# Performance work log

Hardware: AMD Instinct MI355X
Metric: run time of the kernel (lower is better)

## Reference

```python
import jax, jax.numpy as jnp
import numpy as np

EMB_DIM = 300
TEMPERATURE = 0.01
REWEIGHT = True
N = 8192
NUM_GROUPS = 100


def setup_inputs() -> dict:
    key = jax.random.key(0)
    ks = jax.random.split(key, 6)
    s = 1.0 / np.sqrt(EMB_DIM)
    x = jax.random.normal(ks[0], (N, EMB_DIM), dtype=jnp.float32)
    W1 = jax.random.normal(ks[1], (EMB_DIM, EMB_DIM), dtype=jnp.float32) * s
    b1 = jnp.zeros((EMB_DIM,), dtype=jnp.float32)
    W2 = jax.random.normal(ks[2], (EMB_DIM, EMB_DIM), dtype=jnp.float32) * s
    b2 = jnp.zeros((EMB_DIM,), dtype=jnp.float32)
    # labels in [1, 100]: all > 0 so the group_y>0 filter keeps every row
    labels = jax.random.randint(ks[3], (N,), 1, NUM_GROUPS + 1, dtype=jnp.int32)
    return {"x": x, "W1": W1, "b1": b1, "W2": W2, "b2": b2, "labels": labels}


def reference(x, W1, b1, W2, b2, labels):
    # projector: Linear -> ReLU -> Linear
    h = jax.nn.relu(x @ W1 + b1) @ W2 + b2
    # L2 normalize rows
    f = h / jnp.linalg.norm(h, axis=1, keepdims=True)
    # pairwise similarity / temperature, row-max subtracted (detached)
    logits = (f @ f.T) / TEMPERATURE                      # [N, N]
    logits = logits - jax.lax.stop_gradient(jnp.max(logits, axis=1, keepdims=True))

    lab = labels[:, None]
    mask = (lab == lab.T).astype(logits.dtype)            # same-group mask
    logits_mask = 1.0 - jnp.eye(mask.shape[0], dtype=logits.dtype)  # drop diagonal
    mask = mask * logits_mask

    # rows with at least one positive (torch filters these; we weight instead)
    pos_count = jnp.sum(mask, axis=1)                     # [N]
    valid = pos_count > 0

    if REWEIGHT:
        pos_m = logits_mask * mask
        neg_m = logits_mask * (1.0 - mask)
        pos_sum = jnp.sum(pos_m, axis=1, keepdims=True)
        neg_sum = jnp.sum(neg_m, axis=1, keepdims=True)
        log_pos = jnp.where(pos_sum > 0, jnp.log(jnp.maximum(pos_sum, 1.0)), 0.0)
        log_neg = jnp.where(neg_sum > 0, jnp.log(jnp.maximum(neg_sum, 1.0)), 0.0)
        logits = (logits - log_pos) * pos_m + (logits - log_neg) * neg_m

    exp_logits = jnp.exp(logits) * logits_mask
    log_prob = logits - jnp.log(jnp.sum(exp_logits, axis=1, keepdims=True))
    mean_log_prob_pos = jnp.sum(mask * log_prob, axis=1) / jnp.where(valid, pos_count, 1.0)
    validf = valid.astype(logits.dtype)
    loss = -TEMPERATURE * jnp.sum(mean_log_prob_pos * validf) / jnp.sum(validf)
    return loss
```

## Files before the change

### kernel.cpp

```cpp
#include <hip/hip_runtime.h>
#include <hip/hip_bf16.h>


#define N_ROWS 8192
#define D_PAD 320
#define NG 100
#define TEMP 0.01f
#define NSPLIT 32
#define JCHUNK (N_ROWS / NSPLIT)
#define LOG2E100 144.2695041f

typedef short short8v __attribute__((ext_vector_type(8)));
typedef float float4v __attribute__((ext_vector_type(4)));

__device__ __forceinline__ short f2bf(float f) {
  union { __hip_bfloat16 h; short s; } u;
  u.h = __float2bfloat16(f);
  return u.s;
}

__global__ __launch_bounds__(256) void setup_kernel(
    const float* __restrict__ W1, const float* __restrict__ W2,
    const int* __restrict__ labels,
    __hip_bfloat16* __restrict__ w1t, __hip_bfloat16* __restrict__ w2t,
    int* __restrict__ counts)
{
  __shared__ int hc[NG + 1];
  int b = blockIdx.x, tid = threadIdx.x;
  if (b < 800) {
    int isW2 = (b >= 400);
    int idx = (b - (isW2 ? 400 : 0)) * 256 + tid;
    const float* W = isW2 ? W2 : W1;
    __hip_bfloat16* dst = isW2 ? w2t : w1t;
    int n = idx / D_PAD, k = idx - n * D_PAD;
    float v = (n < 300 && k < 300) ? W[(size_t)k * 300 + n] : 0.0f;
    dst[idx] = __float2bfloat16(v);
  } else {
    if (tid <= NG) hc[tid] = 0;
    __syncthreads();
    int row = (b - 800) * 256 + tid;
    atomicAdd(&hc[labels[row]], 1);
    __syncthreads();
    if (tid <= NG && hc[tid] > 0) atomicAdd(&counts[tid], hc[tid]);
  }
}

__global__ __launch_bounds__(256, 2) void mlp_fused_kernel(
    const float* __restrict__ x, const __hip_bfloat16* __restrict__ w1t,
    const __hip_bfloat16* __restrict__ w2t, const float* __restrict__ b1,
    const float* __restrict__ b2, __hip_bfloat16* __restrict__ fb)
{
  __shared__ __align__(16) short Ws[64 * D_PAD];
  __shared__ __align__(16) short H1[64 * D_PAD];
  int tid = threadIdx.x;
  int lane = tid & 63, wave = tid >> 6;
  int g = lane >> 4, lc = lane & 15, sw = lc & 7;
  int i0 = blockIdx.x * 64;

  short8v afr[10];
  {
    const float* xp = x + (size_t)(i0 + wave * 16 + lc) * 300;
#pragma unroll
    for (int kk = 0; kk < 10; ++kk) {
      int k0 = kk * 32 + g * 8;
      short8v v;
      if (k0 + 8 <= 300) {
        float4 a = *(const float4*)(xp + k0);
        float4 c = *(const float4*)(xp + k0 + 4);
        v[0] = f2bf(a.x); v[1] = f2bf(a.y); v[2] = f2bf(a.z); v[3] = f2bf(a.w);
        v[4] = f2bf(c.x); v[5] = f2bf(c.y); v[6] = f2bf(c.z); v[7] = f2bf(c.w);
      } else if (k0 < 300) {
        float4 a = *(const float4*)(xp + k0);
        v[0] = f2bf(a.x); v[1] = f2bf(a.y); v[2] = f2bf(a.z); v[3] = f2bf(a.w);
        v[4] = 0; v[5] = 0; v[6] = 0; v[7] = 0;
      } else {
        v = short8v{0, 0, 0, 0, 0, 0, 0, 0};
      }
      afr[kk] = v;
    }
  }

  for (int c = 0; c < 5; ++c) {
    __syncthreads();
    {
      const int4* src = (const int4*)w1t;
      int4* dst = (int4*)Ws;
#pragma unroll
      for (int t = 0; t < 10; ++t) {
        int e = tid + t * 256;
        int r = e / 40, q = e - r * 40;
        dst[r * 40 + (q ^ (r & 7))] = src[(size_t)(c * 64 + r) * 40 + q];
      }
    }
    __syncthreads();
    for (int js = 0; js < 4; ++js) {
      float4v acc = {0.f, 0.f, 0.f, 0.f};
      const short* rowp = Ws + (js * 16 + lc) * D_PAD;
#pragma unroll
      for (int kk = 0; kk < 10; ++kk) {
        short8v bf = *(const short8v*)(rowp + (((g + 4 * kk) ^ sw) << 3));
        acc = __builtin_amdgcn_mfma_f32_16x16x32_bf16(afr[kk], bf, acc, 0, 0, 0);
      }
      int n = c * 64 + js * 16 + lc;
      float bv = (n < 300) ? b1[n] : 0.0f;
#pragma unroll
      for (int r = 0; r < 4; ++r) {
        int row = wave * 16 + g * 4 + r;
        int q = n >> 3;
        H1[row * D_PAD + ((q ^ (row & 7)) << 3) + (n & 7)] =
            f2bf(fmaxf(acc[r] + bv, 0.0f));
      }
    }
  }
  __syncthreads();

  short8v hfr[10];
  {
    const short* rp = H1 + (wave * 16 + lc) * D_PAD;
#pragma unroll
    for (int kk = 0; kk < 10; ++kk)
      hfr[kk] = *(const short8v*)(rp + (((g + 4 * kk) ^ sw) << 3));
  }

  float4v h2a[5][4];
  for (int c = 0; c < 5; ++c) {
    __syncthreads();
    {
      const int4* src = (const int4*)w2t;
      int4* dst = (int4*)Ws;
#pragma unroll
      for (int t = 0; t < 10; ++t) {
        int e = tid + t * 256;
        int r = e / 40, q = e - r * 40;
        dst[r * 40 + (q ^ (r & 7))] = src[(size_t)(c * 64 + r) * 40 + q];
      }
    }
    __syncthreads();
#pragma unroll
    for (int js = 0; js < 4; ++js) {
      float4v acc = {0.f, 0.f, 0.f, 0.f};
      const short* rowp = Ws + (js * 16 + lc) * D_PAD;
#pragma unroll
      for (int kk = 0; kk < 10; ++kk) {
        short8v bf = *(const short8v*)(rowp + (((g + 4 * kk) ^ sw) << 3));
        acc = __builtin_amdgcn_mfma_f32_16x16x32_bf16(hfr[kk], bf, acc, 0, 0, 0);
      }
      int n = c * 64 + js * 16 + lc;
      float bv = (n < 300) ? b2[n] : 0.0f;
#pragma unroll
      for (int r = 0; r < 4; ++r) acc[r] += bv;
      h2a[c][js] = acc;
    }
  }

  float ssq[4] = {0.f, 0.f, 0.f, 0.f};
#pragma unroll
  for (int c = 0; c < 5; ++c)
#pragma unroll
    for (int js = 0; js < 4; ++js)
#pragma unroll
      for (int r = 0; r < 4; ++r) ssq[r] = fmaf(h2a[c][js][r], h2a[c][js][r], ssq[r]);
  for (int m = 1; m < 16; m <<= 1)
#pragma unroll
    for (int r = 0; r < 4; ++r) ssq[r] += __shfl_xor(ssq[r], m, 64);
  float inv[4];
#pragma unroll
  for (int r = 0; r < 4; ++r) inv[r] = rsqrtf(ssq[r]);
#pragma unroll
  for (int c = 0; c < 5; ++c)
#pragma unroll
    for (int js = 0; js < 4; ++js) {
      int n = c * 64 + js * 16 + lc;
#pragma unroll
      for (int r = 0; r < 4; ++r) {
        int row = i0 + wave * 16 + g * 4 + r;
        fb[(size_t)row * D_PAD + n] = __float2bfloat16(h2a[c][js][r] * inv[r]);
      }
    }
}

__global__ __launch_bounds__(256) void group_kernel(
    const __hip_bfloat16* __restrict__ Fb, const int* __restrict__ labels,
    float* __restrict__ sPar, float* __restrict__ sAar)
{
  __shared__ __align__(16) short Bs[64 * D_PAD];
  __shared__ int memb[256];
  __shared__ int cnt;
  const short* Fs = (const short*)Fb;
  int tid = threadIdx.x;
  int lane = tid & 63, wave = tid >> 6;
  int g = lane >> 4, lc = lane & 15, sw = lc & 7;
  int grp = blockIdx.x + 1;
  if (tid == 0) cnt = 0;
  __syncthreads();
  for (int i = tid; i < N_ROWS; i += 256)
    if (labels[i] == grp) { int p = atomicAdd(&cnt, 1); if (p < 256) memb[p] = i; }
  __syncthreads();
  int c = cnt > 256 ? 256 : cnt;
  int nt = (c + 63) >> 6;
  for (int it = 0; it < nt; ++it) {
    short8v afr[10];
    {
      int islot = it * 64 + wave * 16 + lc;
      int arow = memb[islot < c ? islot : 0];
      const short* ap = Fs + (size_t)arow * D_PAD + g * 8;
#pragma unroll
      for (int kk = 0; kk < 10; ++kk) afr[kk] = *(const short8v*)(ap + kk * 32);
    }
    int iglobr[4]; bool ivalid[4];
    for (int r = 0; r < 4; ++r) {
      int islot = it * 64 + wave * 16 + g * 4 + r;
      ivalid[r] = islot < c;
      iglobr[r] = memb[islot < c ? islot : 0];
    }
    float sp[4] = {}, sa[4] = {};
    for (int jt = 0; jt < nt; ++jt) {
      __syncthreads();
      {
        const int4* src = (const int4*)Fs;
        int4* dst = (int4*)Bs;
#pragma unroll
        for (int t = 0; t < 10; ++t) {
          int e = tid + t * 256;
          int r = e / 40, q = e - r * 40;
          int jslot = jt * 64 + r;
          int grow = memb[jslot < c ? jslot : 0];
          dst[r * 40 + (q ^ (r & 7))] = src[(size_t)grow * 40 + q];
        }
      }
      __syncthreads();
      for (int js = 0; js < 4; ++js) {
        float4v acc = {0.f, 0.f, 0.f, 0.f};
        const short* rowp = Bs + (js * 16 + lc) * D_PAD;
#pragma unroll
        for (int kk = 0; kk < 10; ++kk) {
          short8v bf = *(const short8v*)(rowp + (((g + 4 * kk) ^ sw) << 3));
          acc = __builtin_amdgcn_mfma_f32_16x16x32_bf16(afr[kk], bf, acc, 0, 0, 0);
        }
        int jslot = jt * 64 + js * 16 + lc;
        bool jv = jslot < c;
        int jglob = memb[jslot < c ? jslot : 0];
#pragma unroll
        for (int r = 0; r < 4; ++r) {
          float a = acc[r];
          float e = exp2f(fmaf(a, LOG2E100, -LOG2E100));
          bool ok = jv && ivalid[r] && (jglob != iglobr[r]);
          sp[r] += ok ? e : 0.f;
          sa[r] += ok ? a : 0.f;
        }
      }
    }
    for (int m = 1; m < 16; m <<= 1)
      for (int r = 0; r < 4; ++r) {
        sp[r] += __shfl_xor(sp[r], m, 64);
        sa[r] += __shfl_xor(sa[r], m, 64);
      }
    if (lc == 0)
      for (int r = 0; r < 4; ++r)
        if (ivalid[r]) { sPar[iglobr[r]] = sp[r]; sAar[iglobr[r]] = sa[r]; }
  }
}

__global__ __launch_bounds__(256, 2) void pairwise_kernel(
    const __hip_bfloat16* __restrict__ Fb, float* __restrict__ partE)
{
  __shared__ __align__(16) short Bs[64 * D_PAD];
  const short* Fs = (const short*)Fb;
  int tid = threadIdx.x;
  int lane = tid & 63, wave = tid >> 6;
  int g = lane >> 4, lc = lane & 15, sw = lc & 7;
  int i0 = blockIdx.x * 128;
  int split = blockIdx.y;
  int jstart = split * JCHUNK;

  short8v afr[2][10];
  for (int s = 0; s < 2; ++s) {
    const short* ap = Fs + (size_t)(i0 + s * 64 + wave * 16 + lc) * D_PAD + g * 8;
#pragma unroll
    for (int kk = 0; kk < 10; ++kk) afr[s][kk] = *(const short8v*)(ap + kk * 32);
  }
  float sE[2][4] = {};

  for (int jt = 0; jt < JCHUNK / 64; ++jt) {
    int jb = jstart + jt * 64;
    __syncthreads();
    {
      const int4* src = (const int4*)Fs;
      int4* dst = (int4*)Bs;
#pragma unroll
      for (int t = 0; t < 10; ++t) {
        int e = tid + t * 256;
        int r = e / 40, q = e - r * 40;
        dst[r * 40 + (q ^ (r & 7))] = src[(size_t)(jb + r) * 40 + q];
      }
    }
    __syncthreads();
    for (int js = 0; js < 4; ++js) {
      float4v acc0 = {0.f, 0.f, 0.f, 0.f}, acc1 = {0.f, 0.f, 0.f, 0.f};
      const short* rowp = Bs + (js * 16 + lc) * D_PAD;
#pragma unroll
      for (int kk = 0; kk < 10; ++kk) {
        short8v bf = *(const short8v*)(rowp + (((g + 4 * kk) ^ sw) << 3));
        acc0 = __builtin_amdgcn_mfma_f32_16x16x32_bf16(afr[0][kk], bf, acc0, 0, 0, 0);
        acc1 = __builtin_amdgcn_mfma_f32_16x16x32_bf16(afr[1][kk], bf, acc1, 0, 0, 0);
      }
#pragma unroll
      for (int s = 0; s < 2; ++s) {
        float4v acc = s ? acc1 : acc0;
        bool dtile = (jb == i0 + s * 64) && (js == wave);
#pragma unroll
        for (int r = 0; r < 4; ++r) {
          float e = exp2f(fmaf(acc[r], LOG2E100, -LOG2E100));
          if (dtile && lc == g * 4 + r) e = 0.0f;
          sE[s][r] += e;
        }
      }
    }
  }
  for (int m = 1; m < 16; m <<= 1)
    for (int s = 0; s < 2; ++s)
      for (int r = 0; r < 4; ++r) sE[s][r] += __shfl_xor(sE[s][r], m, 64);
  if (lc == 0)
    for (int s = 0; s < 2; ++s)
      for (int r = 0; r < 4; ++r)
        partE[split * N_ROWS + i0 + s * 64 + wave * 16 + g * 4 + r] = sE[s][r];
}

__global__ __launch_bounds__(256) void final_a_kernel(
    const float* __restrict__ partE, const float* __restrict__ sPar,
    const float* __restrict__ sAar, const int* __restrict__ counts,
    const int* __restrict__ labels, float* __restrict__ blk)
{
  int tid = threadIdx.x;
  int i = blockIdx.x * 256 + tid;
  float sE = 0.f;
  for (int s = 0; s < NSPLIT; ++s) sE += partE[s * N_ROWS + i];
  float M = 0.f, V = 0.f;
  int pc = counts[labels[i]] - 1;
  if (pc > 0) {
    float P = sPar[i], A = sAar[i];
    float Q = sE - P;
    float pcf = (float)pc, ncf = (float)(N_ROWS - 1 - pc);
    float Z = P / pcf + Q / ncf;
    M = 100.0f * A / pcf - 100.0f - logf(pcf) - logf(Z);
    V = 1.f;
  }
  __shared__ float rm[256], rv[256];
  rm[tid] = M; rv[tid] = V;
  __syncthreads();
  for (int s2 = 128; s2 > 0; s2 >>= 1) {
    if (tid < s2) { rm[tid] += rm[tid + s2]; rv[tid] += rv[tid + s2]; }
    __syncthreads();
  }
  if (tid == 0) { blk[blockIdx.x] = rm[0]; blk[32 + blockIdx.x] = rv[0]; }
}

__global__ void final_b_kernel(const float* __restrict__ blk, float* __restrict__ out)
{
  int lane = threadIdx.x;
  float m = (lane < 32) ? blk[lane] : 0.f;
  float v = (lane < 32) ? blk[32 + lane] : 0.f;
  for (int s = 1; s < 32; s <<= 1) { m += __shfl_xor(m, s, 64); v += __shfl_xor(v, s, 64); }
  if (lane == 0) out[0] = (v > 0.f) ? (-TEMP * m / v) : 0.f;
}

extern "C" void kernel_launch(void* const* d_in, const int* in_sizes, int n_in,
                              void* d_out, int out_size, void* d_ws, size_t ws_size,
                              hipStream_t stream)
{
  const float* x  = (const float*)d_in[0];
  const float* W1 = (const float*)d_in[1];
  const float* b1 = (const float*)d_in[2];
  const float* W2 = (const float*)d_in[3];
  const float* b2 = (const float*)d_in[4];
  const int* labels = (const int*)d_in[5];

  char* ws = (char*)d_ws;
  __hip_bfloat16* fb  = (__hip_bfloat16*)(ws);
  __hip_bfloat16* w1t = (__hip_bfloat16*)(ws + 5242880);
  __hip_bfloat16* w2t = (__hip_bfloat16*)(ws + 5447680);
  int*         counts = (int*)(ws + 5652480);
  float*        partE = (float*)(ws + 5652992);
  float*        sPar  = (float*)(ws + 6701568);
  float*        sAar  = (float*)(ws + 6734336);
  float*        blk   = (float*)(ws + 6767104);

  hipMemsetAsync(counts, 0, (NG + 1) * sizeof(int), stream);
  setup_kernel<<<832, 256, 0, stream>>>(W1, W2, labels, w1t, w2t, counts);
  mlp_fused_kernel<<<N_ROWS / 64, 256, 0, stream>>>(x, w1t, w2t, b1, b2, fb);
  group_kernel<<<NG, 256, 0, stream>>>(fb, labels, sPar, sAar);
  pairwise_kernel<<<dim3(N_ROWS / 128, NSPLIT), 256, 0, stream>>>(fb, partE);
  final_a_kernel<<<32, 256, 0, stream>>>(partE, sPar, sAar, counts, labels, blk);
  final_b_kernel<<<1, 64, 0, stream>>>(blk, (float*)d_out);
}
```

Before: 174.1 us.

## Double-buffer pairwise B tiles via direct global-to-LDS loads and widen row block

The pairwise kernel now stages each 64-row B tile straight from global memory into LDS with global_load_lds. Two LDS buffers let the next tile's load overlap the MFMA and exp work on the current tile. The XOR swizzle moves from the LDS write address to the global read address, so the stored layout stays the same. The row block per workgroup also grows from 128 to 256, so each LDS B fragment feeds four MFMA chains instead of two and the grid is halved. In exchange, register use rises (40 A-fragment vectors per lane) and LDS doubles to about 80KB per block, which may limit occupancy.

```diff
diff --git a/kernel.cpp b/kernel.cpp
--- a/kernel.cpp
+++ b/kernel.cpp
@@ -8,6 +8,7 @@
 #define TEMP 0.01f
 #define NSPLIT 32
 #define JCHUNK (N_ROWS / NSPLIT)
+#define IBLK 256
 #define LOG2E100 144.2695041f
 
 typedef short short8v __attribute__((ext_vector_type(8)));
@@ -261,52 +262,71 @@
   }
 }
 
+__device__ __forceinline__ void stage_tile(const short* __restrict__ Fs, int jb,
+                                           short* __restrict__ buf, int tid)
+{
+  int lane = tid & 63;
+  int wbase = tid - lane;
+#pragma unroll
+  for (int t = 0; t < 10; ++t) {
+    int ebase = t * 256 + wbase;
+    int e = ebase + lane;
+    int r = e / 40, qs = e - r * 40;
+    int q = qs ^ (r & 7);
+    const int4* gsrc = (const int4*)(Fs + (size_t)(jb + r) * D_PAD) + q;
+    __builtin_amdgcn_global_load_lds(
+        (const __attribute__((address_space(1))) void*)gsrc,
+        (__attribute__((address_space(3))) void*)((int4*)buf + ebase),
+        16, 0, 0);
+  }
+}
+
 __global__ __launch_bounds__(256, 2) void pairwise_kernel(
     const __hip_bfloat16* __restrict__ Fb, float* __restrict__ partE)
 {
-  __shared__ __align__(16) short Bs[64 * D_PAD];
+  __shared__ __align__(16) short Bs[2][64 * D_PAD];
   const short* Fs = (const short*)Fb;
   int tid = threadIdx.x;
   int lane = tid & 63, wave = tid >> 6;
   int g = lane >> 4, lc = lane & 15, sw = lc & 7;
-  int i0 = blockIdx.x * 128;
+  int i0 = blockIdx.x * IBLK;
   int split = blockIdx.y;
   int jstart = split * JCHUNK;
 
-  short8v afr[2][10];
-  for (int s = 0; s < 2; ++s) {
+  short8v afr[4][10];
+#pragma unroll
+  for (int s = 0; s < 4; ++s) {
     const short* ap = Fs + (size_t)(i0 + s * 64 + wave * 16 + lc) * D_PAD + g * 8;
 #pragma unroll
     for (int kk = 0; kk < 10; ++kk) afr[s][kk] = *(const short8v*)(ap + kk * 32);
   }
-  float sE[2][4] = {};
+  float sE[4][4] = {};
+
+  stage_tile(Fs, jstart, &Bs[0][0], tid);
+  __syncthreads();
 
   for (int jt = 0; jt < JCHUNK / 64; ++jt) {
     int jb = jstart + jt * 64;
-    __syncthreads();
-    {
-      const int4* src = (const int4*)Fs;
-      int4* dst = (int4*)Bs;
-#pragma unroll
-      for (int t = 0; t < 10; ++t) {
-        int e = tid + t * 256;
-        int r = e / 40, q = e - r * 40;
-        dst[r * 40 + (q ^ (r & 7))] = src[(size_t)(jb + r) * 40 + q];
-      }
-    }
-    __syncthreads();
+    int cur = jt & 1;
+    if (jt + 1 < JCHUNK / 64)
+      stage_tile(Fs, jb + 64, &Bs[cur ^ 1][0], tid);
+
+    const short* bufp = &Bs[cur][0];
     for (int js = 0; js < 4; ++js) {
       float4v acc0 = {0.f, 0.f, 0.f, 0.f}, acc1 = {0.f, 0.f, 0.f, 0.f};
-      const short* rowp = Bs + (js * 16 + lc) * D_PAD;
+      float4v acc2 = {0.f, 0.f, 0.f, 0.f}, acc3 = {0.f, 0.f, 0.f, 0.f};
+      const short* rowp = bufp + (js * 16 + lc) * D_PAD;
 #pragma unroll
       for (int kk = 0; kk < 10; ++kk) {
         short8v bf = *(const short8v*)(rowp + (((g + 4 * kk) ^ sw) << 3));
         acc0 = __builtin_amdgcn_mfma_f32_16x16x32_bf16(afr[0][kk], bf, acc0, 0, 0, 0);
         acc1 = __builtin_amdgcn_mfma_f32_16x16x32_bf16(afr[1][kk], bf, acc1, 0, 0, 0);
-      }
-#pragma unroll
-      for (int s = 0; s < 2; ++s) {
-        float4v acc = s ? acc1 : acc0;
+        acc2 = __builtin_amdgcn_mfma_f32_16x16x32_bf16(afr[2][kk], bf, acc2, 0, 0, 0);
+        acc3 = __builtin_amdgcn_mfma_f32_16x16x32_bf16(afr[3][kk], bf, acc3, 0, 0, 0);
+      }
+#pragma unroll
+      for (int s = 0; s < 4; ++s) {
+        float4v acc = (s == 0) ? acc0 : (s == 1) ? acc1 : (s == 2) ? acc2 : acc3;
         bool dtile = (jb == i0 + s * 64) && (js == wave);
 #pragma unroll
         for (int r = 0; r < 4; ++r) {
@@ -316,12 +336,18 @@
         }
       }
     }
-  }
+    __syncthreads();
+  }
+
   for (int m = 1; m < 16; m <<= 1)
-    for (int s = 0; s < 2; ++s)
+#pragma unroll
+    for (int s = 0; s < 4; ++s)
+#pragma unroll
       for (int r = 0; r < 4; ++r) sE[s][r] += __shfl_xor(sE[s][r], m, 64);
   if (lc == 0)
-    for (int s = 0; s < 2; ++s)
+#pragma unroll
+    for (int s = 0; s < 4; ++s)
+#pragma unroll
       for (int r = 0; r < 4; ++r)
         partE[split * N_ROWS + i0 + s * 64 + wave * 16 + g * 4 + r] = sE[s][r];
 }
@@ -389,7 +415,7 @@
   setup_kernel<<<832, 256, 0, stream>>>(W1, W2, labels, w1t, w2t, counts);
   mlp_fused_kernel<<<N_ROWS / 64, 256, 0, stream>>>(x, w1t, w2t, b1, b2, fb);
   group_kernel<<<NG, 256, 0, stream>>>(fb, labels, sPar, sAar);
-  pairwise_kernel<<<dim3(N_ROWS / 128, NSPLIT), 256, 0, stream>>>(fb, partE);
+  pairwise_kernel<<<dim3(N_ROWS / IBLK, NSPLIT), 256, 0, stream>>>(fb, partE);
   final_a_kernel<<<32, 256, 0, stream>>>(partE, sPar, sAar, counts, labels, blk);
   final_b_kernel<<<1, 64, 0, stream>>>(blk, (float*)d_out);
 }
```

Result: slower. 204.4 us (+17.4%).
